# Kernel tuning notes

Hardware: AMD Instinct MI355X
Metric: run time of the kernel (lower is better)

## Reference

```python
import jax, jax.numpy as jnp
import numpy as np

L, D, H, B, N = 4, 1024, 16, 4, 1024
DK = D // H
BN_EPS = 1e-5


def conv1x1(x, W, b):
    # x: (B, C_in, N), W: (C_out, C_in), b: (C_out,)
    return jnp.einsum('oc,bcn->bon', W, x) + b[:, None]


def setup_inputs() -> dict:
    key = jax.random.key(0)
    ks = jax.random.split(key, 17)
    s = 0.02
    inp = {
        'motion_feats': jax.random.normal(ks[0], (B, D, N), dtype=jnp.float32),
        'Wq': jax.random.normal(ks[1], (L, D, D), dtype=jnp.float32) * s,
        'bq': jax.random.normal(ks[2], (L, D), dtype=jnp.float32) * s,
        'Wk': jax.random.normal(ks[3], (L, D, D), dtype=jnp.float32) * s,
        'bk': jax.random.normal(ks[4], (L, D), dtype=jnp.float32) * s,
        'Wv': jax.random.normal(ks[5], (L, D, D), dtype=jnp.float32) * s,
        'bv': jax.random.normal(ks[6], (L, D), dtype=jnp.float32) * s,
        'Wm': jax.random.normal(ks[7], (L, D, D), dtype=jnp.float32) * s,
        'bm': jax.random.normal(ks[8], (L, D), dtype=jnp.float32) * s,
        'Wp1': jax.random.normal(ks[9], (L, 2 * D, 2 * D), dtype=jnp.float32) * s,
        'bp1': jax.random.normal(ks[10], (L, 2 * D), dtype=jnp.float32) * s,
        'bn_gamma': 1.0 + 0.1 * jax.random.normal(ks[11], (L, 2 * D), dtype=jnp.float32),
        'bn_beta': 0.1 * jax.random.normal(ks[12], (L, 2 * D), dtype=jnp.float32),
        'bn_mean': 0.1 * jax.random.normal(ks[13], (L, 2 * D), dtype=jnp.float32),
        'bn_var': 0.5 + jax.random.uniform(ks[14], (L, 2 * D), dtype=jnp.float32),
        'Wp2': jax.random.normal(ks[15], (L, D, 2 * D), dtype=jnp.float32) * s,
        'bp2': jnp.zeros((L, D), dtype=jnp.float32),  # init.constant_(bias, 0)
    }
    return inp


def _mha_layer(x, Wq, bq, Wk, bk, Wv, bv, Wm, bm, Wp1, bp1, g, bta, mu, var, Wp2, bp2):
    # x: (B, D, N)
    q = conv1x1(x, Wq, bq).reshape(B, DK, H, N)
    k = conv1x1(x, Wk, bk).reshape(B, DK, H, N)
    v = conv1x1(x, Wv, bv).reshape(B, DK, H, N)
    scores = jnp.einsum('bdhn,bdhm->bhnm', q, k) / jnp.sqrt(jnp.float32(DK))
    w = jax.nn.softmax(scores, axis=-1)
    attn = jnp.einsum('bhnm,bdhm->bdhn', w, v).reshape(B, D, N)
    merged = conv1x1(attn, Wm, bm)
    h = jnp.concatenate([merged, x], axis=1)  # (B, 2D, N)
    h = conv1x1(h, Wp1, bp1)
    # BatchNorm1d in eval mode (running stats)
    h = g[:, None] * (h - mu[:, None]) * jax.lax.rsqrt(var[:, None] + BN_EPS) + bta[:, None]
    h = jax.nn.relu(h)
    return conv1x1(h, Wp2, bp2)


def reference(motion_feats, Wq, bq, Wk, bk, Wv, bv, Wm, bm, Wp1, bp1,
              bn_gamma, bn_beta, bn_mean, bn_var, Wp2, bp2):
    x = motion_feats
    for l in range(L):
        attn_out = _mha_layer(x, Wq[l], bq[l], Wk[l], bk[l], Wv[l], bv[l],
                              Wm[l], bm[l], Wp1[l], bp1[l],
                              bn_gamma[l], bn_beta[l], bn_mean[l], bn_var[l],
                              Wp2[l], bp2[l])
        x = x + attn_out
    return x
```

## Files before the change

kernel.cpp:

```cpp
#include <hip/hip_runtime.h>

typedef unsigned short u16;
typedef __attribute__((ext_vector_type(8))) short bf16x8;
typedef __attribute__((ext_vector_type(4))) float f32x4;

#define B_ 4
#define D_ 1024
#define N_ 1024
#define H_ 16
#define DK_ 64

__device__ inline float bf2f(u16 x) {
    union { unsigned u; float f; } c; c.u = ((unsigned)x) << 16; return c.f;
}
__device__ inline u16 f2bf(float f) {
    union { float f; unsigned u; } c; c.f = f;
    unsigned r = c.u + 0x7fff + ((c.u >> 16) & 1);
    return (u16)(r >> 16);
}

#if __has_builtin(__builtin_amdgcn_exp2f)
#define EXP2(x) __builtin_amdgcn_exp2f(x)
#else
#define EXP2(x) __expf((x) * 0.6931471805599453f)
#endif

__device__ inline bf16x8 load8(const void* p, size_t idx, int fl) {
    if (!fl) return *(const bf16x8*)((const u16*)p + idx);
    const float* fp = (const float*)p + idx;
    f32x4 a = *(const f32x4*)fp;
    f32x4 b = *(const f32x4*)(fp + 4);
    bf16x8 r;
    #pragma unroll
    for (int j = 0; j < 4; ++j) {
        ((u16*)&r)[j]     = f2bf(a[j]);
        ((u16*)&r)[4 + j] = f2bf(b[j]);
    }
    return r;
}

__global__ __launch_bounds__(256) void k_cvt(
    const float* __restrict__ src, u16* __restrict__ dst, int n8)
{
    int i = blockIdx.x * 256 + threadIdx.x;
    if (i < n8) {
        const f32x4* s = (const f32x4*)src;
        f32x4 a = s[2 * i], b = s[2 * i + 1];
        bf16x8 r;
        #pragma unroll
        for (int j = 0; j < 4; ++j) {
            ((u16*)&r)[j]     = f2bf(a[j]);
            ((u16*)&r)[4 + j] = f2bf(b[j]);
        }
        ((bf16x8*)dst)[i] = r;
    }
}

__device__ __forceinline__ void gload16(const u16* g, u16* l) {
    __builtin_amdgcn_global_load_lds(
        (const __attribute__((address_space(1))) void*)g,
        (__attribute__((address_space(3))) void*)l, 16, 0, 0);
}

template<int ROWS>
__device__ __forceinline__ void stage_rows(const u16* __restrict__ g, int ld,
                                           int k0, u16* L, int wave)
{
    #pragma unroll
    for (int i = 0; i < ROWS / 64; ++i)
        gload16(g + (size_t)(i * 64) * ld + k0, L + i * 2048 + wave * 512);
}

template<int N>
__device__ __forceinline__ void waitcnt_vm() {
    if constexpr (N == 0)      asm volatile("s_waitcnt vmcnt(0)" ::: "memory");
    else if constexpr (N == 3) asm volatile("s_waitcnt vmcnt(3)" ::: "memory");
    else if constexpr (N == 4) asm volatile("s_waitcnt vmcnt(4)" ::: "memory");
    else if constexpr (N == 6) asm volatile("s_waitcnt vmcnt(6)" ::: "memory");
    else if constexpr (N == 8) asm volatile("s_waitcnt vmcnt(8)" ::: "memory");
}

template<int MT, int NT>
__device__ inline void gemm_bf16(const u16* __restrict__ A, int lda,
                                 const u16* __restrict__ Bt, size_t eoff,
                                 int ldb, int K, int m0, int n0,
                                 u16* lds, f32x4 acc[MT/32][NT/32])
{
    constexpr int FM = MT / 32, FN = NT / 32;
    constexpr int TSZ = (MT + NT) * 32;
    constexpr int NL  = MT / 64 + NT / 64;
    const int tid  = threadIdx.x;
    const int wave = tid >> 6, lane = tid & 63;
    const int quad = lane >> 4, l15 = lane & 15;
    const int wm = (wave >> 1) * (MT / 2);
    const int wn = (wave & 1) * (NT / 2);

    const u16* ga = A + (size_t)(m0 + (tid >> 2)) * lda + ((tid & 3) << 3);
    const u16* gb = Bt + eoff + (size_t)(n0 + (tid >> 2)) * ldb + ((tid & 3) << 3);

    stage_rows<MT>(ga, lda, 0, lds, wave);
    stage_rows<NT>(gb, ldb, 0, lds + MT * 32, wave);
    if (K > 32) {
        stage_rows<MT>(ga, lda, 32, lds + TSZ, wave);
        stage_rows<NT>(gb, ldb, 32, lds + TSZ + MT * 32, wave);
    }

    int b0 = 0;
    for (int k0 = 0; k0 < K - 32; k0 += 32) {
        waitcnt_vm<NL>();
        __builtin_amdgcn_s_barrier();

        const u16* La = lds + b0 * TSZ;
        const u16* Lb = La + MT * 32;
        bf16x8 af[FM], bv[FN];
        #pragma unroll
        for (int f = 0; f < FM; ++f)
            af[f] = *(const bf16x8*)&La[(wm + f * 16 + l15) * 32 + quad * 8];
        #pragma unroll
        for (int f = 0; f < FN; ++f)
            bv[f] = *(const bf16x8*)&Lb[(wn + f * 16 + l15) * 32 + quad * 8];

        if (k0 + 64 < K) {
            int b2 = b0 + 2; if (b2 >= 3) b2 -= 3;
            u16* Nx = lds + b2 * TSZ;
            stage_rows<MT>(ga, lda, k0 + 64, Nx, wave);
            stage_rows<NT>(gb, ldb, k0 + 64, Nx + MT * 32, wave);
        }

        #pragma unroll
        for (int fm = 0; fm < FM; ++fm)
            #pragma unroll
            for (int fn = 0; fn < FN; ++fn)
                acc[fm][fn] = __builtin_amdgcn_mfma_f32_16x16x32_bf16(
                    af[fm], bv[fn], acc[fm][fn], 0, 0, 0);

        b0 = (b0 == 2) ? 0 : b0 + 1;
    }

    waitcnt_vm<0>();
    __builtin_amdgcn_s_barrier();
    {
        const u16* La = lds + b0 * TSZ;
        const u16* Lb = La + MT * 32;
        bf16x8 af[FM], bv[FN];
        #pragma unroll
        for (int f = 0; f < FM; ++f)
            af[f] = *(const bf16x8*)&La[(wm + f * 16 + l15) * 32 + quad * 8];
        #pragma unroll
        for (int f = 0; f < FN; ++f)
            bv[f] = *(const bf16x8*)&Lb[(wn + f * 16 + l15) * 32 + quad * 8];
        #pragma unroll
        for (int fm = 0; fm < FM; ++fm)
            #pragma unroll
            for (int fn = 0; fn < FN; ++fn)
                acc[fm][fn] = __builtin_amdgcn_mfma_f32_16x16x32_bf16(
                    af[fm], bv[fn], acc[fm][fn], 0, 0, 0);
    }
    __syncthreads();
}

template<int MT, int NT>
__device__ inline void gemm_core(const u16* __restrict__ A, int lda,
                                 const void* __restrict__ Bt, size_t eoff,
                                 int ldb, int fl,
                                 int K, int m0, int n0,
                                 u16* lds, f32x4 acc[MT/32][NT/32])
{
    constexpr int FM = MT / 32, FN = NT / 32;
    constexpr int CA = MT * 4 / 256, CB = NT * 4 / 256;
    const int tid  = threadIdx.x;
    const int wave = tid >> 6, lane = tid & 63;
    const int quad = lane >> 4, l15 = lane & 15;
    const int wm = (wave >> 1) * (MT / 2);
    const int wn = (wave & 1) * (NT / 2);

    int arow[CA], acol[CA], brow[CB], bcol[CB];
    #pragma unroll
    for (int i = 0; i < CA; ++i) { int x = tid + i * 256; arow[i] = x >> 2; acol[i] = (x & 3) << 3; }
    #pragma unroll
    for (int i = 0; i < CB; ++i) { int x = tid + i * 256; brow[i] = x >> 2; bcol[i] = (x & 3) << 3; }

    bf16x8 pa[CA], pb[CB];
    #pragma unroll
    for (int i = 0; i < CA; ++i)
        pa[i] = *(const bf16x8*)(A + (size_t)(m0 + arow[i]) * lda + acol[i]);
    #pragma unroll
    for (int i = 0; i < CB; ++i)
        pb[i] = load8(Bt, eoff + (size_t)(n0 + brow[i]) * ldb + bcol[i], fl);

    int buf = 0;
    for (int k0 = 0; k0 < K; k0 += 32) {
        u16* La = lds + buf * ((MT + NT) * 40);
        u16* Lb = La + MT * 40;
        #pragma unroll
        for (int i = 0; i < CA; ++i) *(bf16x8*)&La[arow[i] * 40 + acol[i]] = pa[i];
        #pragma unroll
        for (int i = 0; i < CB; ++i) *(bf16x8*)&Lb[brow[i] * 40 + bcol[i]] = pb[i];
        __syncthreads();

        if (k0 + 32 < K) {
            #pragma unroll
            for (int i = 0; i < CA; ++i)
                pa[i] = *(const bf16x8*)(A + (size_t)(m0 + arow[i]) * lda + k0 + 32 + acol[i]);
            #pragma unroll
            for (int i = 0; i < CB; ++i)
                pb[i] = load8(Bt, eoff + (size_t)(n0 + brow[i]) * ldb + k0 + 32 + bcol[i], fl);
        }

        bf16x8 af[FM], bv[FN];
        #pragma unroll
        for (int f = 0; f < FM; ++f)
            af[f] = *(bf16x8*)&La[(wm + f * 16 + l15) * 40 + quad * 8];
        #pragma unroll
        for (int f = 0; f < FN; ++f)
            bv[f] = *(bf16x8*)&Lb[(wn + f * 16 + l15) * 40 + quad * 8];
        #pragma unroll
        for (int fm = 0; fm < FM; ++fm)
            #pragma unroll
            for (int fn = 0; fn < FN; ++fn)
                acc[fm][fn] = __builtin_amdgcn_mfma_f32_16x16x32_bf16(
                    af[fm], bv[fn], acc[fm][fn], 0, 0, 0);
        buf ^= 1;
    }
}

#define EPI_SETUP \
    const int tid = threadIdx.x; \
    const int wave = tid >> 6, lane = tid & 63; \
    const int quad = lane >> 4, l15 = lane & 15;

__global__ __launch_bounds__(256) void k_qkv(
    const u16* __restrict__ xb,
    const void* __restrict__ Wq, const void* __restrict__ Wk, const void* __restrict__ Wv,
    const float* __restrict__ bq, const float* __restrict__ bk, const float* __restrict__ bv,
    int fl, u16* __restrict__ qh, u16* __restrict__ kh, u16* __restrict__ vt)
{
    __shared__ u16 lds[3 * (128 + 128) * 32];
    int mat = blockIdx.z;
    const void* W     = mat == 0 ? Wq : (mat == 1 ? Wk : Wv);
    const float* bias = mat == 0 ? bq : (mat == 1 ? bk : bv);
    int m0 = blockIdx.x * 128, n0 = blockIdx.y * 128;

    f32x4 acc[4][4];
    #pragma unroll
    for (int i = 0; i < 4; ++i)
        #pragma unroll
        for (int j = 0; j < 4; ++j) acc[i][j] = f32x4{0.f, 0.f, 0.f, 0.f};

    if (fl) gemm_core<128, 128>(xb, D_, W, 0, D_, 1, D_, m0, n0, lds, acc);
    else    gemm_bf16<128, 128>(xb, D_, (const u16*)W, 0, D_, D_, m0, n0, lds, acc);

    EPI_SETUP
    const int wm = (wave >> 1) * 64, wn = (wave & 1) * 64;
    #pragma unroll
    for (int fm = 0; fm < 4; ++fm)
        #pragma unroll
        for (int fn = 0; fn < 4; ++fn) {
            int n = n0 + wn + fn * 16 + l15;
            float bz = bias[n];
            int h = n & 15, dk = n >> 4;
            #pragma unroll
            for (int r = 0; r < 4; ++r) {
                int m = m0 + wm + fm * 16 + quad * 4 + r;
                int b = m >> 10, pos = m & 1023;
                int bh = b * H_ + h;
                u16 o = f2bf(acc[fm][fn][r] + bz);
                if (mat == 0) {
                    qh[(((size_t)bh * N_ + pos) * DK_ + dk)] = o;
                } else if (mat == 1) {
                    size_t kidx = (((size_t)bh * 64 + (pos >> 4)) << 10)
                                + ((dk >> 5) << 9) + (((dk >> 3) & 3) << 7)
                                + ((pos & 15) << 3) + (dk & 7);
                    kh[kidx] = o;
                } else {
                    size_t vidx = (((size_t)bh * 32 + (pos >> 5)) << 11)
                                + ((dk >> 4) << 9) + (((pos >> 3) & 3) << 7)
                                + ((dk & 15) << 3) + (pos & 7);
                    vt[vidx] = o;
                }
            }
        }
}

__global__ __launch_bounds__(64) void k_flash(
    const u16* __restrict__ qh, const u16* __restrict__ kh,
    const u16* __restrict__ vt, u16* __restrict__ at)
{
    __shared__ u16 P[16 * 136];

    const int bh = blockIdx.y, b = bh >> 4, h = bh & 15;
    const int lane = threadIdx.x;
    const int quad = lane >> 4, l15 = lane & 15;
    const int q0 = blockIdx.x * 16;

    const u16* Q  = qh + (size_t)bh * N_ * DK_;
    const u16* Kf = kh + ((size_t)bh << 16);
    const u16* Vf = vt + ((size_t)bh << 16);

    bf16x8 qf[2];
    #pragma unroll
    for (int kk = 0; kk < 2; ++kk)
        qf[kk] = *(const bf16x8*)&Q[(size_t)(q0 + l15) * DK_ + kk * 32 + quad * 8];

    f32x4 acc_o[4];
    #pragma unroll
    for (int j = 0; j < 4; ++j) acc_o[j] = f32x4{0.f, 0.f, 0.f, 0.f};
    float mrow[4], lrow[4];
    #pragma unroll
    for (int r = 0; r < 4; ++r) { mrow[r] = -1e30f; lrow[r] = 0.f; }

    const float c = 0.18033688011112042f;

    #pragma unroll 2
    for (int mt = 0; mt < 8; ++mt) {
        f32x4 s[8];
        #pragma unroll
        for (int j = 0; j < 8; ++j) s[j] = f32x4{0.f, 0.f, 0.f, 0.f};
        #pragma unroll
        for (int kk = 0; kk < 2; ++kk) {
            bf16x8 kf[8];
            #pragma unroll
            for (int fn = 0; fn < 8; ++fn)
                kf[fn] = *(const bf16x8*)&Kf[((size_t)(mt * 8 + fn) << 10)
                                             + (kk << 9) + (quad << 7) + (l15 << 3)];
            #pragma unroll
            for (int fn = 0; fn < 8; ++fn)
                s[fn] = __builtin_amdgcn_mfma_f32_16x16x32_bf16(
                    qf[kk], kf[fn], s[fn], 0, 0, 0);
        }

        #pragma unroll
        for (int r = 0; r < 4; ++r) {
            float mx = s[0][r];
            #pragma unroll
            for (int fn = 1; fn < 8; ++fn) mx = fmaxf(mx, s[fn][r]);
            #pragma unroll
            for (int o = 1; o < 16; o <<= 1)
                mx = fmaxf(mx, __shfl_xor(mx, o, 64));
            float mn = fmaxf(mrow[r], mx);
            float al = EXP2((mrow[r] - mn) * c);
            float nmc = -mn * c;
            float rs = 0.f;
            #pragma unroll
            for (int fn = 0; fn < 8; ++fn) {
                float p = EXP2(fmaf(s[fn][r], c, nmc));
                s[fn][r] = p;
                rs += p;
            }
            #pragma unroll
            for (int o = 1; o < 16; o <<= 1)
                rs += __shfl_xor(rs, o, 64);
            lrow[r] = al * lrow[r] + rs;
            mrow[r] = mn;
            #pragma unroll
            for (int fn = 0; fn < 4; ++fn) acc_o[fn][r] *= al;
        }

        #pragma unroll
        for (int fn = 0; fn < 8; ++fn)
            #pragma unroll
            for (int r = 0; r < 4; ++r)
                P[(quad * 4 + r) * 136 + fn * 16 + l15] = f2bf(s[fn][r]);

        #pragma unroll
        for (int ks = 0; ks < 4; ++ks) {
            bf16x8 vf[4];
            #pragma unroll
            for (int fn = 0; fn < 4; ++fn)
                vf[fn] = *(const bf16x8*)&Vf[((size_t)(mt * 4 + ks) << 11)
                                             + (fn << 9) + (quad << 7) + (l15 << 3)];
            bf16x8 pf = *(bf16x8*)&P[l15 * 136 + ks * 32 + quad * 8];
            #pragma unroll
            for (int fn = 0; fn < 4; ++fn)
                acc_o[fn] = __builtin_amdgcn_mfma_f32_16x16x32_bf16(
                    pf, vf[fn], acc_o[fn], 0, 0, 0);
        }
    }

    #pragma unroll
    for (int r = 0; r < 4; ++r) {
        float inv = 1.f / lrow[r];
        int pos = q0 + quad * 4 + r;
        #pragma unroll
        for (int fn = 0; fn < 4; ++fn) {
            int dk = fn * 16 + l15;
            at[((size_t)(b * N_ + pos)) * D_ + dk * 16 + h] =
                f2bf(acc_o[fn][r] * inv);
        }
    }
}

__global__ __launch_bounds__(256) void k_merged(
    const u16* __restrict__ at, const void* __restrict__ Wm,
    const float* __restrict__ bm, int fl, u16* __restrict__ mg)
{
    __shared__ u16 lds[3 * (64 + 128) * 32];
    int m0 = blockIdx.x * 64, n0 = blockIdx.y * 128;

    f32x4 acc[2][4];
    #pragma unroll
    for (int i = 0; i < 2; ++i)
        #pragma unroll
        for (int j = 0; j < 4; ++j) acc[i][j] = f32x4{0.f, 0.f, 0.f, 0.f};

    if (fl) gemm_core<64, 128>(at, D_, Wm, 0, D_, 1, D_, m0, n0, lds, acc);
    else    gemm_bf16<64, 128>(at, D_, (const u16*)Wm, 0, D_, D_, m0, n0, lds, acc);

    EPI_SETUP
    const int wm = (wave >> 1) * 32, wn = (wave & 1) * 64;
    #pragma unroll
    for (int fm = 0; fm < 2; ++fm)
        #pragma unroll
        for (int fn = 0; fn < 4; ++fn) {
            int n = n0 + wn + fn * 16 + l15;
            float bz = bm[n];
            #pragma unroll
            for (int r = 0; r < 4; ++r) {
                int m = m0 + wm + fm * 16 + quad * 4 + r;
                mg[(size_t)m * D_ + n] = f2bf(acc[fm][fn][r] + bz);
            }
        }
}

__global__ __launch_bounds__(256) void k_p1(
    const u16* __restrict__ mg, const u16* __restrict__ xb,
    const void* __restrict__ Wp1, int fl,
    const float* __restrict__ bp1, const float* __restrict__ gam,
    const float* __restrict__ bet, const float* __restrict__ mu,
    const float* __restrict__ var, u16* __restrict__ h2)
{
    __shared__ u16 lds[3 * (128 + 128) * 32];
    int m0 = blockIdx.x * 128, n0 = blockIdx.y * 128;

    f32x4 acc[4][4];
    #pragma unroll
    for (int i = 0; i < 4; ++i)
        #pragma unroll
        for (int j = 0; j < 4; ++j) acc[i][j] = f32x4{0.f, 0.f, 0.f, 0.f};

    if (fl) {
        gemm_core<128, 128>(mg, D_, Wp1, 0,    2048, 1, D_, m0, n0, lds, acc);
        gemm_core<128, 128>(xb, D_, Wp1, 1024, 2048, 1, D_, m0, n0, lds, acc);
    } else {
        gemm_bf16<128, 128>(mg, D_, (const u16*)Wp1, 0,    2048, D_, m0, n0, lds, acc);
        gemm_bf16<128, 128>(xb, D_, (const u16*)Wp1, 1024, 2048, D_, m0, n0, lds, acc);
    }

    EPI_SETUP
    const int wm = (wave >> 1) * 64, wn = (wave & 1) * 64;
    #pragma unroll
    for (int fm = 0; fm < 4; ++fm)
        #pragma unroll
        for (int fn = 0; fn < 4; ++fn) {
            int n = n0 + wn + fn * 16 + l15;
            float bz = bp1[n];
            float sc = gam[n] * rsqrtf(var[n] + 1e-5f);
            float mn = mu[n], be = bet[n];
            #pragma unroll
            for (int r = 0; r < 4; ++r) {
                int m = m0 + wm + fm * 16 + quad * 4 + r;
                float y = (acc[fm][fn][r] + bz - mn) * sc + be;
                h2[(size_t)m * 2048 + n] = f2bf(fmaxf(y, 0.f));
            }
        }
}

__global__ __launch_bounds__(256) void k_p2(
    const u16* __restrict__ h2, const void* __restrict__ Wp2,
    const float* __restrict__ bp2, int fl,
    float* __restrict__ xf, u16* __restrict__ xb)
{
    __shared__ u16 lds[3 * (64 + 128) * 32];
    int m0 = blockIdx.x * 64, n0 = blockIdx.y * 128;

    f32x4 acc[2][4];
    #pragma unroll
    for (int i = 0; i < 2; ++i)
        #pragma unroll
        for (int j = 0; j < 4; ++j) acc[i][j] = f32x4{0.f, 0.f, 0.f, 0.f};

    if (fl) gemm_core<64, 128>(h2, 2048, Wp2, 0, 2048, 1, 2048, m0, n0, lds, acc);
    else    gemm_bf16<64, 128>(h2, 2048, (const u16*)Wp2, 0, 2048, 2048, m0, n0, lds, acc);

    EPI_SETUP
    const int wm = (wave >> 1) * 32, wn = (wave & 1) * 64;
    #pragma unroll
    for (int fm = 0; fm < 2; ++fm)
        #pragma unroll
        for (int fn = 0; fn < 4; ++fn) {
            int n = n0 + wn + fn * 16 + l15;
            float bz = bp2[n];
            #pragma unroll
            for (int r = 0; r < 4; ++r) {
                int m = m0 + wm + fm * 16 + quad * 4 + r;
                size_t ad = (size_t)m * D_ + n;
                float nv = xf[ad] + acc[fm][fn][r] + bz;
                xf[ad] = nv;
                xb[ad] = f2bf(nv);
            }
        }
}

__global__ __launch_bounds__(256) void k_tin(
    const float* __restrict__ mo, float* __restrict__ xf, u16* __restrict__ xb)
{
    __shared__ float t[32][33];
    int b = blockIdx.z;
    int p0 = blockIdx.x * 32, c0 = blockIdx.y * 32;
    int tx = threadIdx.x & 31, ty = threadIdx.x >> 5;
    const float* src = mo + ((size_t)b * D_ + c0) * N_ + p0;
    #pragma unroll
    for (int k = 0; k < 4; ++k)
        t[ty + k * 8][tx] = src[(size_t)(ty + k * 8) * N_ + tx];
    __syncthreads();
    size_t base = ((size_t)b * N_ + p0) * D_ + c0;
    #pragma unroll
    for (int k = 0; k < 4; ++k) {
        float v = t[tx][ty + k * 8];
        xf[base + (size_t)(ty + k * 8) * D_ + tx] = v;
        xb[base + (size_t)(ty + k * 8) * D_ + tx] = f2bf(v);
    }
}

__global__ __launch_bounds__(256) void k_tout(
    const float* __restrict__ xf, float* __restrict__ out)
{
    __shared__ float t[32][33];
    int b = blockIdx.z;
    int c0 = blockIdx.x * 32, p0 = blockIdx.y * 32;
    int tx = threadIdx.x & 31, ty = threadIdx.x >> 5;
    const float* src = xf + ((size_t)b * N_ + p0) * D_ + c0;
    #pragma unroll
    for (int k = 0; k < 4; ++k)
        t[ty + k * 8][tx] = src[(size_t)(ty + k * 8) * D_ + tx];
    __syncthreads();
    float* dst = out + ((size_t)b * D_ + c0) * N_ + p0;
    #pragma unroll
    for (int k = 0; k < 4; ++k)
        dst[(size_t)(ty + k * 8) * N_ + tx] = t[tx][ty + k * 8];
}

extern "C" void kernel_launch(void* const* d_in, const int* in_sizes, int n_in,
                              void* d_out, int out_size, void* d_ws, size_t ws_size,
                              hipStream_t stream)
{
    const float* mo  = (const float*)d_in[0];
    const float* Wqf = (const float*)d_in[1];
    const float* bq  = (const float*)d_in[2];
    const float* Wkf = (const float*)d_in[3];
    const float* bk  = (const float*)d_in[4];
    const float* Wvf = (const float*)d_in[5];
    const float* bv  = (const float*)d_in[6];
    const float* Wmf = (const float*)d_in[7];
    const float* bm  = (const float*)d_in[8];
    const float* Wp1f= (const float*)d_in[9];
    const float* bp1 = (const float*)d_in[10];
    const float* gam = (const float*)d_in[11];
    const float* bet = (const float*)d_in[12];
    const float* mu  = (const float*)d_in[13];
    const float* var = (const float*)d_in[14];
    const float* Wp2f= (const float*)d_in[15];
    const float* bp2 = (const float*)d_in[16];

    char* ws = (char*)d_ws;
    float* xf = (float*)ws;
    u16* xb   = (u16*)(ws + (16ull << 20));
    u16* qh   = (u16*)(ws + (24ull << 20));
    u16* kh   = (u16*)(ws + (32ull << 20));
    u16* vt   = (u16*)(ws + (40ull << 20));
    u16* at   = (u16*)(ws + (48ull << 20));
    u16* mg   = qh;
    u16* h2   = kh;
    u16* wb   = (u16*)(ws + (56ull << 20));

    const size_t S1 = 1048576;
    const size_t SP1 = 4194304;
    const size_t SP2 = 2097152;
    const size_t OQ = 0, OK4 = 4 * S1, OV = 8 * S1, OM = 12 * S1,
                 OP1 = 16 * S1, OP2 = OP1 + 4 * SP1;

    int mode;
    if (ws_size >= (137ull << 20)) mode = 2;
    else if (ws_size >= (77ull << 20)) mode = 1;
    else mode = 0;
    const int fl = (mode == 0) ? 1 : 0;

    dim3 blk(256);
    if (mode == 2) {
        k_cvt<<<2048, blk, 0, stream>>>(Wqf,  wb + OQ,  524288);
        k_cvt<<<2048, blk, 0, stream>>>(Wkf,  wb + OK4, 524288);
        k_cvt<<<2048, blk, 0, stream>>>(Wvf,  wb + OV,  524288);
        k_cvt<<<2048, blk, 0, stream>>>(Wmf,  wb + OM,  524288);
        k_cvt<<<8192, blk, 0, stream>>>(Wp1f, wb + OP1, 2097152);
        k_cvt<<<4096, blk, 0, stream>>>(Wp2f, wb + OP2, 1048576);
    }

    k_tin<<<dim3(32, 32, 4), blk, 0, stream>>>(mo, xf, xb);

    for (int l = 0; l < 4; ++l) {
        const void *pWq, *pWk, *pWv, *pWm, *pWp1, *pWp2;
        if (mode == 2) {
            pWq  = wb + OQ  + (size_t)l * S1;
            pWk  = wb + OK4 + (size_t)l * S1;
            pWv  = wb + OV  + (size_t)l * S1;
            pWm  = wb + OM  + (size_t)l * S1;
            pWp1 = wb + OP1 + (size_t)l * SP1;
            pWp2 = wb + OP2 + (size_t)l * SP2;
        } else if (mode == 1) {
            k_cvt<<<512,  blk, 0, stream>>>(Wqf  + l * S1,  wb,               131072);
            k_cvt<<<512,  blk, 0, stream>>>(Wkf  + l * S1,  wb + S1,          131072);
            k_cvt<<<512,  blk, 0, stream>>>(Wvf  + l * S1,  wb + 2 * S1,      131072);
            k_cvt<<<512,  blk, 0, stream>>>(Wmf  + l * S1,  wb + 3 * S1,      131072);
            k_cvt<<<2048, blk, 0, stream>>>(Wp1f + l * SP1, wb + 4 * S1,      524288);
            k_cvt<<<1024, blk, 0, stream>>>(Wp2f + l * SP2, wb + 4 * S1 + SP1, 262144);
            pWq = wb; pWk = wb + S1; pWv = wb + 2 * S1; pWm = wb + 3 * S1;
            pWp1 = wb + 4 * S1; pWp2 = wb + 4 * S1 + SP1;
        } else {
            pWq  = Wqf  + l * S1;
            pWk  = Wkf  + l * S1;
            pWv  = Wvf  + l * S1;
            pWm  = Wmf  + l * S1;
            pWp1 = Wp1f + l * SP1;
            pWp2 = Wp2f + l * SP2;
        }

        k_qkv<<<dim3(32, 8, 3), blk, 0, stream>>>(
            xb, pWq, pWk, pWv, bq + l * D_, bk + l * D_, bv + l * D_, fl, qh, kh, vt);
        k_flash<<<dim3(64, 64), dim3(64), 0, stream>>>(qh, kh, vt, at);
        k_merged<<<dim3(64, 8), blk, 0, stream>>>(at, pWm, bm + l * D_, fl, mg);
        k_p1<<<dim3(32, 16), blk, 0, stream>>>(
            mg, xb, pWp1, fl, bp1 + l * 2048, gam + l * 2048, bet + l * 2048,
            mu + l * 2048, var + l * 2048, h2);
        k_p2<<<dim3(64, 8), blk, 0, stream>>>(
            h2, pWp2, bp2 + l * D_, fl, xf, xb);
    }
    k_tout<<<dim3(32, 32, 4), blk, 0, stream>>>(xf, (float*)d_out);
}
```

Measured before the change: 1.188 ms.

## Stage QKV and attention outputs through LDS for vectorized coalesced stores

The QKV epilogue now writes results into a swizzled LDS tile and then emits 16-byte vector stores to the head-major Q/K/V layouts, instead of scattered 2-byte global stores. Q gets a new chunked layout that the flash kernel reads directly. The flash kernel's output is likewise staged through LDS and stored head-contiguous, and the merge weight is pre-permuted on conversion (k_cvtperm) to match that new attention layout. This targets uncoalesced write traffic, at the cost of extra LDS passes, barriers and a strided per-call weight permutation.

Measured after the change: 992.6 us. -16.5%, faster.

```diff
diff --git a/kernel.cpp b/kernel.cpp
--- a/kernel.cpp
+++ b/kernel.cpp
@@ -54,6 +54,19 @@
         }
         ((bf16x8*)dst)[i] = r;
     }
+}
+
+__global__ __launch_bounds__(256) void k_cvtperm(
+    const float* __restrict__ src, u16* __restrict__ dst)
+{
+    int i = blockIdx.x * 256 + threadIdx.x;
+    int n = i >> 7, c8 = i & 127;
+    int h = c8 >> 3, dkb = (c8 & 7) * 8;
+    bf16x8 r;
+    #pragma unroll
+    for (int e = 0; e < 8; ++e)
+        ((u16*)&r)[e] = f2bf(src[(size_t)n * 1024 + (size_t)(dkb + e) * 16 + h]);
+    *(bf16x8*)&dst[(size_t)n * 1024 + h * 64 + dkb] = r;
 }
 
 __device__ __forceinline__ void gload16(const u16* g, u16* l) {
@@ -229,13 +242,17 @@
     const int wave = tid >> 6, lane = tid & 63; \
     const int quad = lane >> 4, l15 = lane & 15;
 
+__device__ __forceinline__ int swz(int off) {
+    return off ^ (((off >> 10) & 7) << 3);
+}
+
 __global__ __launch_bounds__(256) void k_qkv(
     const u16* __restrict__ xb,
     const void* __restrict__ Wq, const void* __restrict__ Wk, const void* __restrict__ Wv,
     const float* __restrict__ bq, const float* __restrict__ bk, const float* __restrict__ bv,
     int fl, u16* __restrict__ qh, u16* __restrict__ kh, u16* __restrict__ vt)
 {
-    __shared__ u16 lds[3 * (128 + 128) * 32];
+    __shared__ __align__(16) u16 lds[3 * (128 + 128) * 32];
     int mat = blockIdx.z;
     const void* W     = mat == 0 ? Wq : (mat == 1 ? Wk : Wv);
     const float* bias = mat == 0 ? bq : (mat == 1 ? bk : bv);
@@ -251,56 +268,83 @@
     else    gemm_bf16<128, 128>(xb, D_, (const u16*)W, 0, D_, D_, m0, n0, lds, acc);
 
     EPI_SETUP
+    __syncthreads();
     const int wm = (wave >> 1) * 64, wn = (wave & 1) * 64;
+    const int b = m0 >> 10, pos0 = m0 & 1023;
+    const int dk0 = n0 >> 4;
+
     #pragma unroll
     for (int fm = 0; fm < 4; ++fm)
         #pragma unroll
         for (int fn = 0; fn < 4; ++fn) {
-            int n = n0 + wn + fn * 16 + l15;
-            float bz = bias[n];
-            int h = n & 15, dk = n >> 4;
+            int n_l = wn + fn * 16 + l15;
+            float bz = bias[n0 + n_l];
             #pragma unroll
             for (int r = 0; r < 4; ++r) {
-                int m = m0 + wm + fm * 16 + quad * 4 + r;
-                int b = m >> 10, pos = m & 1023;
-                int bh = b * H_ + h;
+                int m_l = wm + fm * 16 + quad * 4 + r;
                 u16 o = f2bf(acc[fm][fn][r] + bz);
-                if (mat == 0) {
-                    qh[(((size_t)bh * N_ + pos) * DK_ + dk)] = o;
-                } else if (mat == 1) {
-                    size_t kidx = (((size_t)bh * 64 + (pos >> 4)) << 10)
-                                + ((dk >> 5) << 9) + (((dk >> 3) & 3) << 7)
-                                + ((pos & 15) << 3) + (dk & 7);
-                    kh[kidx] = o;
-                } else {
-                    size_t vidx = (((size_t)bh * 32 + (pos >> 5)) << 11)
-                                + ((dk >> 4) << 9) + (((pos >> 3) & 3) << 7)
-                                + ((dk & 15) << 3) + (pos & 7);
-                    vt[vidx] = o;
-                }
+                int off;
+                if (mat == 0)
+                    off = ((n_l & 15) << 10) + (m_l << 3) + (n_l >> 4);
+                else if (mat == 1)
+                    off = (((n_l & 15) * 8 + (m_l >> 4)) << 7)
+                        + ((m_l & 15) << 3) + (n_l >> 4);
+                else
+                    off = (((n_l & 15) * 4 + (m_l >> 5)) << 8)
+                        + (((m_l >> 3) & 3) << 6) + ((n_l >> 4) << 3) + (m_l & 7);
+                lds[swz(off)] = o;
             }
         }
+    __syncthreads();
+
+    #pragma unroll
+    for (int j = 0; j < 8; ++j) {
+        int flat = j * 2048 + tid * 8;
+        bf16x8 v = *(const bf16x8*)&lds[swz(flat)];
+        if (mat == 0) {
+            int h = flat >> 10;
+            int bh = b * 16 + h;
+            size_t ga = (((size_t)(bh * 8 + (n0 >> 7)) * 1024 + pos0) << 3)
+                      + (flat & 1023);
+            *(bf16x8*)&qh[ga] = v;
+        } else if (mat == 1) {
+            int run = flat >> 7, h = run >> 3, g = run & 7;
+            int bh = b * 16 + h;
+            size_t base = (((size_t)bh * 64 + (pos0 >> 4) + g) << 10)
+                        + ((size_t)(dk0 >> 5) << 9)
+                        + ((size_t)((dk0 >> 3) & 3) << 7);
+            *(bf16x8*)&kh[base + (flat & 127)] = v;
+        } else {
+            int chunk = flat >> 8, h = chunk >> 2, m5 = chunk & 3;
+            int bh = b * 16 + h;
+            size_t base = (((size_t)bh * 32 + (pos0 >> 5) + m5) << 11)
+                        + ((size_t)(dk0 >> 4) << 9)
+                        + ((size_t)((flat >> 6) & 3) << 7)
+                        + ((size_t)(dk0 & 8) << 3);
+            *(bf16x8*)&vt[base + (flat & 63)] = v;
+        }
+    }
 }
 
 __global__ __launch_bounds__(64) void k_flash(
     const u16* __restrict__ qh, const u16* __restrict__ kh,
-    const u16* __restrict__ vt, u16* __restrict__ at)
-{
-    __shared__ u16 P[16 * 136];
+    const u16* __restrict__ vt, u16* __restrict__ at, int alp)
+{
+    __shared__ __align__(16) u16 P[16 * 136];
 
     const int bh = blockIdx.y, b = bh >> 4, h = bh & 15;
     const int lane = threadIdx.x;
     const int quad = lane >> 4, l15 = lane & 15;
     const int q0 = blockIdx.x * 16;
 
-    const u16* Q  = qh + (size_t)bh * N_ * DK_;
     const u16* Kf = kh + ((size_t)bh << 16);
     const u16* Vf = vt + ((size_t)bh << 16);
 
     bf16x8 qf[2];
     #pragma unroll
     for (int kk = 0; kk < 2; ++kk)
-        qf[kk] = *(const bf16x8*)&Q[(size_t)(q0 + l15) * DK_ + kk * 32 + quad * 8];
+        qf[kk] = *(const bf16x8*)&qh[(((size_t)bh * 8 + kk * 4 + quad) * 1024
+                                      + q0 + l15) * 8];
 
     f32x4 acc_o[4];
     #pragma unroll
@@ -377,15 +421,33 @@
         }
     }
 
-    #pragma unroll
-    for (int r = 0; r < 4; ++r) {
-        float inv = 1.f / lrow[r];
-        int pos = q0 + quad * 4 + r;
-        #pragma unroll
-        for (int fn = 0; fn < 4; ++fn) {
-            int dk = fn * 16 + l15;
-            at[((size_t)(b * N_ + pos)) * D_ + dk * 16 + h] =
-                f2bf(acc_o[fn][r] * inv);
+    float inv[4];
+    #pragma unroll
+    for (int r = 0; r < 4; ++r) inv[r] = 1.f / lrow[r];
+
+    if (alp) {
+        #pragma unroll
+        for (int fn = 0; fn < 4; ++fn)
+            #pragma unroll
+            for (int r = 0; r < 4; ++r)
+                P[(quad * 4 + r) * 72 + fn * 16 + l15] = f2bf(acc_o[fn][r] * inv[r]);
+        #pragma unroll
+        for (int j = 0; j < 2; ++j) {
+            int cidx = j * 64 + lane;
+            int pos_l = cidx >> 3, dk8 = cidx & 7;
+            bf16x8 v = *(const bf16x8*)&P[pos_l * 72 + dk8 * 8];
+            *(bf16x8*)&at[((size_t)(b * N_ + q0 + pos_l)) * D_ + h * 64 + dk8 * 8] = v;
+        }
+    } else {
+        #pragma unroll
+        for (int r = 0; r < 4; ++r) {
+            int pos = q0 + quad * 4 + r;
+            #pragma unroll
+            for (int fn = 0; fn < 4; ++fn) {
+                int dk = fn * 16 + l15;
+                at[((size_t)(b * N_ + pos)) * D_ + dk * 16 + h] =
+                    f2bf(acc_o[fn][r] * inv[r]);
+            }
         }
     }
 }
@@ -394,7 +456,7 @@
     const u16* __restrict__ at, const void* __restrict__ Wm,
     const float* __restrict__ bm, int fl, u16* __restrict__ mg)
 {
-    __shared__ u16 lds[3 * (64 + 128) * 32];
+    __shared__ __align__(16) u16 lds[3 * (64 + 128) * 32];
     int m0 = blockIdx.x * 64, n0 = blockIdx.y * 128;
 
     f32x4 acc[2][4];
@@ -429,7 +491,7 @@
     const float* __restrict__ bet, const float* __restrict__ mu,
     const float* __restrict__ var, u16* __restrict__ h2)
 {
-    __shared__ u16 lds[3 * (128 + 128) * 32];
+    __shared__ __align__(16) u16 lds[3 * (128 + 128) * 32];
     int m0 = blockIdx.x * 128, n0 = blockIdx.y * 128;
 
     f32x4 acc[4][4];
@@ -470,7 +532,7 @@
     const float* __restrict__ bp2, int fl,
     float* __restrict__ xf, u16* __restrict__ xb)
 {
-    __shared__ u16 lds[3 * (64 + 128) * 32];
+    __shared__ __align__(16) u16 lds[3 * (64 + 128) * 32];
     int m0 = blockIdx.x * 64, n0 = blockIdx.y * 128;
 
     f32x4 acc[2][4];
@@ -584,13 +646,15 @@
     else if (ws_size >= (77ull << 20)) mode = 1;
     else mode = 0;
     const int fl = (mode == 0) ? 1 : 0;
+    const int alp = (mode != 0);
 
     dim3 blk(256);
     if (mode == 2) {
         k_cvt<<<2048, blk, 0, stream>>>(Wqf,  wb + OQ,  524288);
         k_cvt<<<2048, blk, 0, stream>>>(Wkf,  wb + OK4, 524288);
         k_cvt<<<2048, blk, 0, stream>>>(Wvf,  wb + OV,  524288);
-        k_cvt<<<2048, blk, 0, stream>>>(Wmf,  wb + OM,  524288);
+        for (int l = 0; l < 4; ++l)
+            k_cvtperm<<<512, blk, 0, stream>>>(Wmf + l * S1, wb + OM + l * S1);
         k_cvt<<<8192, blk, 0, stream>>>(Wp1f, wb + OP1, 2097152);
         k_cvt<<<4096, blk, 0, stream>>>(Wp2f, wb + OP2, 1048576);
     }
@@ -610,7 +674,7 @@
             k_cvt<<<512,  blk, 0, stream>>>(Wqf  + l * S1,  wb,               131072);
             k_cvt<<<512,  blk, 0, stream>>>(Wkf  + l * S1,  wb + S1,          131072);
             k_cvt<<<512,  blk, 0, stream>>>(Wvf  + l * S1,  wb + 2 * S1,      131072);
-            k_cvt<<<512,  blk, 0, stream>>>(Wmf  + l * S1,  wb + 3 * S1,      131072);
+            k_cvtperm<<<512, blk, 0, stream>>>(Wmf + l * S1, wb + 3 * S1);
             k_cvt<<<2048, blk, 0, stream>>>(Wp1f + l * SP1, wb + 4 * S1,      524288);
             k_cvt<<<1024, blk, 0, stream>>>(Wp2f + l * SP2, wb + 4 * S1 + SP1, 262144);
             pWq = wb; pWk = wb + S1; pWv = wb + 2 * S1; pWm = wb + 3 * S1;
@@ -626,7 +690,7 @@
 
         k_qkv<<<dim3(32, 8, 3), blk, 0, stream>>>(
             xb, pWq, pWk, pWv, bq + l * D_, bk + l * D_, bv + l * D_, fl, qh, kh, vt);
-        k_flash<<<dim3(64, 64), dim3(64), 0, stream>>>(qh, kh, vt, at);
+        k_flash<<<dim3(64, 64), dim3(64), 0, stream>>>(qh, kh, vt, at, alp);
         k_merged<<<dim3(64, 8), blk, 0, stream>>>(at, pWm, bm + l * D_, fl, mg);
         k_p1<<<dim3(32, 16), blk, 0, stream>>>(
             mg, xb, pWp1, fl, bp1 + l * 2048, gam + l * 2048, bet + l * 2048,
```
